# Kernel optimization log

Hardware: AMD Instinct MI355X
Metric: run time of the kernel (lower is better)

## Reference

```python
import jax, jax.numpy as jnp
import numpy as np

D_MODEL = 2048
N_HEADS = 16
HEAD_DIM = D_MODEL // N_HEADS
D_FF = ((int(8 * D_MODEL / 3) + 64) // 64) * 64  # 5504
B, T = 2, 2048
EPS = 1e-8
NEG = -1e9


def rotate_half(x):
    half = x.shape[-1] // 2
    return jnp.concatenate([-x[..., half:], x[..., :half]], axis=-1)


def apply_rope(x, cos, sin):
    # x: [B,H,T,hd]; cos/sin: [T,hd] -> [1,1,T,hd]
    c = cos[None, None, :, :]
    s = sin[None, None, :, :]
    return x * c + rotate_half(x) * s


def rmsnorm(x, w):
    rms = jnp.sqrt(jnp.mean(x * x, axis=-1, keepdims=True))
    return w * x / (rms + EPS)


def setup_inputs() -> dict:
    key = jax.random.key(0)
    ks = jax.random.split(key, 12)
    x = jax.random.normal(ks[0], (B, T, D_MODEL), dtype=jnp.float32)
    # RoPE tables
    inv_freq = 1.0 / (10000.0 ** (jnp.arange(0, HEAD_DIM, 2, dtype=jnp.float32) / HEAD_DIM))
    pos = jnp.arange(T, dtype=jnp.float32)
    freqs = pos[:, None] * inv_freq[None, :]          # [T, hd/2]
    emb = jnp.concatenate([freqs, freqs], axis=-1)    # [T, hd]
    cos, sin = jnp.cos(emb), jnp.sin(emb)
    # causal additive mask [T,T]
    mask = jnp.where(jnp.tril(jnp.ones((T, T), dtype=bool)), 0.0, NEG).astype(jnp.float32)
    scale = 0.02
    Wq = jax.random.normal(ks[1], (D_MODEL, D_MODEL), dtype=jnp.float32) * scale
    Wk = jax.random.normal(ks[2], (D_MODEL, D_MODEL), dtype=jnp.float32) * scale
    Wv = jax.random.normal(ks[3], (D_MODEL, D_MODEL), dtype=jnp.float32) * scale
    Wo = jax.random.normal(ks[4], (D_MODEL, D_MODEL), dtype=jnp.float32) * scale
    W1 = jax.random.normal(ks[5], (D_FF, D_MODEL), dtype=jnp.float32) * scale
    W2 = jax.random.normal(ks[6], (D_FF, D_MODEL), dtype=jnp.float32) * scale
    Wout = jax.random.normal(ks[7], (D_MODEL, D_FF), dtype=jnp.float32) * scale
    g1 = jnp.ones((D_MODEL,), dtype=jnp.float32)
    g2 = jnp.ones((D_MODEL,), dtype=jnp.float32)
    return {"x": x, "cos": cos, "sin": sin, "mask": mask,
            "g1": g1, "g2": g2, "Wq": Wq, "Wk": Wk, "Wv": Wv, "Wo": Wo,
            "W1": W1, "W2": W2, "Wout": Wout}


def reference(x, cos, sin, mask, g1, g2, Wq, Wk, Wv, Wo, W1, W2, Wout):
    Bb, Tt, Dd = x.shape

    def split_heads(t):  # [B,T,D] -> [B,H,T,hd]
        return t.reshape(Bb, Tt, N_HEADS, HEAD_DIM).transpose(0, 2, 1, 3)

    h = rmsnorm(x, g1)
    Q = apply_rope(split_heads(h @ Wq.T), cos, sin)
    K = apply_rope(split_heads(h @ Wk.T), cos, sin)
    V = split_heads(h @ Wv.T)
    scores = jnp.einsum('bhqd,bhkd->bhqk', Q, K) / jnp.sqrt(jnp.float32(HEAD_DIM))
    scores = scores + mask  # broadcast [T,T] over [B,H,T,T]
    weights = jax.nn.softmax(scores, axis=-1)
    attn = jnp.einsum('bhqk,bhkd->bhqd', weights, V)
    attn = attn.transpose(0, 2, 1, 3).reshape(Bb, Tt, Dd)
    x = x + attn @ Wo.T

    h2 = rmsnorm(x, g2)
    ff = (jax.nn.silu(h2 @ W1.T) * (h2 @ W2.T)) @ Wout.T
    return x + ff
```

## Files before the change

kernel.cpp:

```cpp
#include <hip/hip_runtime.h>


using bf16 = __bf16;
typedef __bf16 bf16x2 __attribute__((ext_vector_type(2)));
typedef __bf16 bf16x8 __attribute__((ext_vector_type(8)));
typedef float f32x4 __attribute__((ext_vector_type(4)));

#define MFMA_BF16(a, b, c) __builtin_amdgcn_mfma_f32_16x16x32_bf16((a), (b), (c), 0, 0, 0)

__device__ __forceinline__ void gld_lds16(const void* g, void* l) {
  __builtin_amdgcn_global_load_lds((const __attribute__((address_space(1))) void*)g,
                                   (__attribute__((address_space(3))) void*)l,
                                   16, 0, 0);
}

__global__ void detect_dtype(const unsigned int* __restrict__ X, int* __restrict__ flag) {
  const int tid = threadIdx.x;
  const unsigned int w = X[tid];
  const unsigned int e_lo = (w >> 7) & 0xFF;
  const unsigned int e_hi = (w >> 23) & 0xFF;
  const bool sane = (e_lo >= 97u && e_lo <= 157u) && (e_hi >= 97u && e_hi <= 157u);
  const unsigned long long m = __ballot(sane);
  if (tid == 0) *flag = (__popcll(m) > 48) ? 1 : 0;
}

__global__ __launch_bounds__(256) void convert_in(const void* __restrict__ src,
                                                  bf16* __restrict__ dst,
                                                  const int* __restrict__ flag) {
  const size_t i = ((size_t)blockIdx.x * 256 + threadIdx.x) * 8;
  if (*flag) {
    *(bf16x8*)(dst + i) = *(const bf16x8*)((const bf16*)src + i);
  } else {
    const float* s = (const float*)src;
    float4 a = *(const float4*)(s + i);
    float4 b = *(const float4*)(s + i + 4);
    bf16x8 o;
    o[0] = (bf16)a.x; o[1] = (bf16)a.y; o[2] = (bf16)a.z; o[3] = (bf16)a.w;
    o[4] = (bf16)b.x; o[5] = (bf16)b.y; o[6] = (bf16)b.z; o[7] = (bf16)b.w;
    *(bf16x8*)(dst + i) = o;
  }
}

__global__ __launch_bounds__(256) void rmsnorm_bf16(const bf16* __restrict__ X,
                                                    const bf16* __restrict__ g,
                                                    bf16* __restrict__ Hout) {
  const int row = blockIdx.x, tid = threadIdx.x;
  const size_t off = (size_t)row * 2048 + tid * 8;
  bf16x8 x8 = *(const bf16x8*)(X + off);
  float v[8];
  float s = 0.f;
#pragma unroll
  for (int j = 0; j < 8; ++j) { v[j] = (float)x8[j]; s += v[j] * v[j]; }
#pragma unroll
  for (int o = 32; o; o >>= 1) s += __shfl_xor(s, o);
  __shared__ float red[4];
  if ((tid & 63) == 0) red[tid >> 6] = s;
  __syncthreads();
  const float tot = red[0] + red[1] + red[2] + red[3];
  const float inv = 1.f / (sqrtf(tot * (1.f / 2048.f)) + 1e-8f);
  bf16x8 g8 = *(const bf16x8*)(g + tid * 8);
  bf16x8 o8;
#pragma unroll
  for (int j = 0; j < 8; ++j) o8[j] = (bf16)((float)g8[j] * v[j] * inv);
  *(bf16x8*)(Hout + off) = o8;
}

__global__ __launch_bounds__(256) void rmsnorm_f32(const float* __restrict__ X,
                                                   const bf16* __restrict__ g,
                                                   bf16* __restrict__ Hout) {
  const int row = blockIdx.x, tid = threadIdx.x;
  const size_t off = (size_t)row * 2048 + tid * 8;
  float4 a0 = *(const float4*)(X + off);
  float4 a1 = *(const float4*)(X + off + 4);
  float v[8] = {a0.x, a0.y, a0.z, a0.w, a1.x, a1.y, a1.z, a1.w};
  float s = 0.f;
#pragma unroll
  for (int j = 0; j < 8; ++j) s += v[j] * v[j];
#pragma unroll
  for (int o = 32; o; o >>= 1) s += __shfl_xor(s, o);
  __shared__ float red[4];
  if ((tid & 63) == 0) red[tid >> 6] = s;
  __syncthreads();
  const float tot = red[0] + red[1] + red[2] + red[3];
  const float inv = 1.f / (sqrtf(tot * (1.f / 2048.f)) + 1e-8f);
  bf16x8 g8 = *(const bf16x8*)(g + tid * 8);
  bf16x8 o8;
#pragma unroll
  for (int j = 0; j < 8; ++j) o8[j] = (bf16)((float)g8[j] * v[j] * inv);
  *(bf16x8*)(Hout + off) = o8;
}

__global__ __launch_bounds__(256) void rope_k(bf16* __restrict__ Q, bf16* __restrict__ Kg,
                                              const bf16* __restrict__ cosb,
                                              const bf16* __restrict__ sinb) {
  const int tid = threadIdx.x;
  const int rr = tid >> 7;
  const int c = tid & 127;
  const int bt = blockIdx.x * 2 + rr;
  const int t = bt & 2047;
  const int h = c >> 3;
  const int d0 = (c & 7) * 8;
  const size_t row = (size_t)bt * 2048;
  const int i0 = h * 128 + d0;
  bf16x8 c0 = *(const bf16x8*)(cosb + t * 128 + d0);
  bf16x8 c1 = *(const bf16x8*)(cosb + t * 128 + d0 + 64);
  bf16x8 s0 = *(const bf16x8*)(sinb + t * 128 + d0);
  bf16x8 s1 = *(const bf16x8*)(sinb + t * 128 + d0 + 64);
  bf16x8 qa = *(const bf16x8*)(Q + row + i0);
  bf16x8 qb = *(const bf16x8*)(Q + row + i0 + 64);
  bf16x8 ka = *(const bf16x8*)(Kg + row + i0);
  bf16x8 kb = *(const bf16x8*)(Kg + row + i0 + 64);
  bf16x8 qo0, qo1, ko0, ko1;
#pragma unroll
  for (int j = 0; j < 8; ++j) {
    float cj0 = (float)c0[j], cj1 = (float)c1[j];
    float sj0 = (float)s0[j], sj1 = (float)s1[j];
    float qaj = (float)qa[j], qbj = (float)qb[j];
    float kaj = (float)ka[j], kbj = (float)kb[j];
    qo0[j] = (bf16)(qaj * cj0 - qbj * sj0);
    qo1[j] = (bf16)(qbj * cj1 + qaj * sj1);
    ko0[j] = (bf16)(kaj * cj0 - kbj * sj0);
    ko1[j] = (bf16)(kbj * cj1 + kaj * sj1);
  }
  *(bf16x8*)(Q + row + i0) = qo0;
  *(bf16x8*)(Q + row + i0 + 64) = qo1;
  *(bf16x8*)(Kg + row + i0) = ko0;
  *(bf16x8*)(Kg + row + i0 + 64) = ko1;
}

template <int EPI>
__global__ __launch_bounds__(256) void gemm_bt(const bf16* __restrict__ A,
                                               const bf16* __restrict__ W,
                                               bf16* __restrict__ Cb, float* __restrict__ Cf,
                                               const bf16* __restrict__ resb,
                                               const float* __restrict__ resf,
                                               const bf16* __restrict__ mulb,
                                               const int* __restrict__ oflag,
                                               int M, int N, int K) {
  __shared__ bf16 As[2][128 * 32];
  __shared__ bf16 Ws[2][128 * 32];
  const int tid = threadIdx.x;
  const int wave = tid >> 6, lane = tid & 63;
  const int quad = lane >> 4, l15 = lane & 15;
  const int wm = wave >> 1, wn = wave & 1;
  const int m0 = blockIdx.y * 128, n0 = blockIdx.x * 128;

  f32x4 acc[4][4];
#pragma unroll
  for (int i = 0; i < 4; ++i)
#pragma unroll
    for (int j = 0; j < 4; ++j) acc[i][j] = {0.f, 0.f, 0.f, 0.f};

  const int srow = lane >> 2;
  const int skk = (lane & 3) * 8;
  const bf16* Ab = A + (size_t)m0 * K;
  const bf16* Wb = W + (size_t)n0 * K;

  auto stage = [&](int buf, int kb) {
    const int k0 = kb << 5;
#pragma unroll
    for (int c = 0; c < 2; ++c) {
      const int r = (wave * 2 + c) * 16 + srow;
      gld_lds16(Ab + (size_t)r * K + k0 + skk, (char*)As[buf] + (wave * 2 + c) * 1024);
      gld_lds16(Wb + (size_t)r * K + k0 + skk, (char*)Ws[buf] + (wave * 2 + c) * 1024);
    }
  };
  auto compute = [&](int buf) {
    bf16x8 af[4], wf[4];
#pragma unroll
    for (int mt = 0; mt < 4; ++mt)
      af[mt] = *(const bf16x8*)&As[buf][(wm * 64 + mt * 16 + l15) * 32 + quad * 8];
#pragma unroll
    for (int nt = 0; nt < 4; ++nt)
      wf[nt] = *(const bf16x8*)&Ws[buf][(wn * 64 + nt * 16 + l15) * 32 + quad * 8];
#pragma unroll
    for (int mt = 0; mt < 4; ++mt)
#pragma unroll
      for (int nt = 0; nt < 4; ++nt)
        acc[mt][nt] = MFMA_BF16(af[mt], wf[nt], acc[mt][nt]);
  };

  const int nk = K >> 5;
  stage(0, 0);
  for (int kb = 0; kb < nk; kb += 2) {
    __syncthreads();
    if (kb + 1 < nk) stage(1, kb + 1);
    compute(0);
    __syncthreads();
    if (kb + 2 < nk) stage(0, kb + 2);
    compute(1);
  }

  const int obf = (EPI == 4 && oflag) ? *oflag : 0;
#pragma unroll
  for (int mt = 0; mt < 4; ++mt) {
#pragma unroll
    for (int nt = 0; nt < 4; ++nt) {
#pragma unroll
      for (int r = 0; r < 4; ++r) {
        const int row = m0 + wm * 64 + mt * 16 + quad * 4 + r;
        const int col = n0 + wn * 64 + nt * 16 + l15;
        const size_t idx = (size_t)row * N + col;
        const float v = acc[mt][nt][r];
        if constexpr (EPI == 0) {
          Cb[idx] = (bf16)v;
        } else if constexpr (EPI == 1) {
          Cf[idx] = v + (float)resb[idx];
        } else if constexpr (EPI == 2) {
          Cb[idx] = (bf16)(v / (1.f + __expf(-v)));
        } else if constexpr (EPI == 3) {
          Cb[idx] = (bf16)((float)mulb[idx] * v);
        } else {
          const float rres = resf[idx] + v;
          if (obf) Cb[idx] = (bf16)rres;
          else     Cf[idx] = rres;
        }
      }
    }
  }
}

__global__ __launch_bounds__(256) void flash_attn(const bf16* __restrict__ Q,
                                                  const bf16* __restrict__ Kg,
                                                  const bf16* __restrict__ Vg,
                                                  bf16* __restrict__ O) {
  __shared__ bf16 Ks[64 * 128];
  __shared__ bf16 Vt[128 * 64];
  __shared__ bf16 Ps[4 * 16 * 64];
  const int tid = threadIdx.x;
  const int wave = tid >> 6, lane = tid & 63;
  const int quad = lane >> 4, l15 = lane & 15;
  const int bh = blockIdx.y;
  const int b = bh >> 4, h = bh & 15;
  const size_t base = (size_t)b * 2048 * 2048 + h * 128;
  const float scale = 0.08838834764831845f;

  const int qt = 31 - (int)blockIdx.x;
  const int q0 = qt * 64;

  bf16x8 qf[4];
  {
    const bf16* qrow = Q + base + (size_t)(q0 + wave * 16 + l15) * 2048;
#pragma unroll
    for (int ks = 0; ks < 4; ++ks) qf[ks] = *(const bf16x8*)(qrow + ks * 32 + quad * 8);
  }

  f32x4 o[8];
#pragma unroll
  for (int i = 0; i < 8; ++i) o[i] = {0.f, 0.f, 0.f, 0.f};
  float m_r[4] = {-1e30f, -1e30f, -1e30f, -1e30f};
  float l_r[4] = {0.f, 0.f, 0.f, 0.f};

  for (int kb = 0; kb <= qt; ++kb) {
    const int k0 = kb * 64;
    __syncthreads();

#pragma unroll
    for (int c = 0; c < 4; ++c) {
      const int ch = tid + 256 * c;
      const int row = ch >> 4;
      const int scb = ((ch & 15) * 16) ^ ((row & 7) << 4);
      gld_lds16((const char*)(Kg + base + (size_t)(k0 + row) * 2048) + scb,
                (char*)Ks + wave * 1024 + c * 4096);
    }
#pragma unroll
    for (int c = 0; c < 2; ++c) {
      const int tau = tid + 256 * c;
      const int kp = tau & 31;
      const int d0 = (tau >> 5) * 8;
      bf16x8 va = *(const bf16x8*)(Vg + base + (size_t)(k0 + 2 * kp) * 2048 + d0);
      bf16x8 vb = *(const bf16x8*)(Vg + base + (size_t)(k0 + 2 * kp + 1) * 2048 + d0);
#pragma unroll
      for (int j = 0; j < 8; ++j) {
        bf16x2 pr = {va[j], vb[j]};
        const int d = d0 + j;
        *(bf16x2*)((char*)Vt + d * 128 + ((4 * kp) ^ ((d & 7) << 4))) = pr;
      }
    }
    __syncthreads();

    f32x4 s[4];
#pragma unroll
    for (int nt = 0; nt < 4; ++nt) {
      s[nt] = {0.f, 0.f, 0.f, 0.f};
      const int krow = nt * 16 + l15;
#pragma unroll
      for (int ks = 0; ks < 4; ++ks) {
        bf16x8 kf = *(const bf16x8*)((char*)Ks + krow * 256 +
                                     ((ks * 64 + quad * 16) ^ ((krow & 7) << 4)));
        s[nt] = MFMA_BF16(qf[ks], kf, s[nt]);
      }
    }

    float sv[4][4];
#pragma unroll
    for (int nt = 0; nt < 4; ++nt) {
#pragma unroll
      for (int r = 0; r < 4; ++r) {
        float v = s[nt][r] * scale;
        const int key = k0 + nt * 16 + l15;
        const int qq = q0 + wave * 16 + quad * 4 + r;
        if (key > qq) v = -1e9f;
        sv[nt][r] = v;
      }
    }

#pragma unroll
    for (int r = 0; r < 4; ++r) {
      float rmax = fmaxf(fmaxf(sv[0][r], sv[1][r]), fmaxf(sv[2][r], sv[3][r]));
#pragma unroll
      for (int off = 1; off < 16; off <<= 1) rmax = fmaxf(rmax, __shfl_xor(rmax, off));
      const float mnew = fmaxf(m_r[r], rmax);
      const float alpha = __expf(m_r[r] - mnew);
      float psum = 0.f;
      const int qrow = quad * 4 + r;
#pragma unroll
      for (int nt = 0; nt < 4; ++nt) {
        const float p = __expf(sv[nt][r] - mnew);
        psum += p;
        *(bf16*)((char*)Ps + wave * 2048 + qrow * 128 +
                 ((2 * (nt * 16 + l15)) ^ ((qrow & 7) << 4))) = (bf16)p;
      }
#pragma unroll
      for (int off = 1; off < 16; off <<= 1) psum += __shfl_xor(psum, off);
      l_r[r] = l_r[r] * alpha + psum;
      m_r[r] = mnew;
#pragma unroll
      for (int nt2 = 0; nt2 < 8; ++nt2) o[nt2][r] *= alpha;
    }

    asm volatile("s_waitcnt lgkmcnt(0)" ::: "memory");

#pragma unroll
    for (int ks2 = 0; ks2 < 2; ++ks2) {
      bf16x8 pf = *(const bf16x8*)((char*)Ps + wave * 2048 + l15 * 128 +
                                   ((ks2 * 64 + quad * 16) ^ ((l15 & 7) << 4)));
#pragma unroll
      for (int nt2 = 0; nt2 < 8; ++nt2) {
        const int drow = nt2 * 16 + l15;
        bf16x8 vf = *(const bf16x8*)((char*)Vt + drow * 128 +
                                     ((ks2 * 64 + quad * 16) ^ ((drow & 7) << 4)));
        o[nt2] = MFMA_BF16(pf, vf, o[nt2]);
      }
    }
  }

#pragma unroll
  for (int nt2 = 0; nt2 < 8; ++nt2) {
#pragma unroll
    for (int r = 0; r < 4; ++r) {
      const int qq = q0 + wave * 16 + quad * 4 + r;
      const int dd = nt2 * 16 + l15;
      O[base + (size_t)qq * 2048 + dd] = (bf16)(o[nt2][r] / l_r[r]);
    }
  }
}

extern "C" void kernel_launch(void* const* d_in, const int* in_sizes, int n_in,
                              void* d_out, int out_size, void* d_ws, size_t ws_size,
                              hipStream_t stream) {
  const void* x_raw = d_in[0];
  const void* cos_raw = d_in[1];
  const void* sin_raw = d_in[2];
  const void* g1_raw = d_in[4];
  const void* g2_raw = d_in[5];
  const void* W_raw[7] = {d_in[6], d_in[7], d_in[8], d_in[9], d_in[10], d_in[11], d_in[12]};

  char* ws = (char*)d_ws;
  const size_t MB = 1048576ull;
  int* flag = (int*)ws;
  bf16* g1c = (bf16*)(ws + 4096);
  bf16* g2c = (bf16*)(ws + 12288);
  bf16* cosc = (bf16*)(ws + 65536);
  bf16* sinc = (bf16*)(ws + 655360);
  bf16* xc   = (bf16*)(ws + 2 * MB);
  bf16* wslot= (bf16*)(ws + 18 * MB);
  bf16* hbuf = (bf16*)(ws + 41 * MB);
  bf16* qbuf = (bf16*)(ws + 57 * MB);
  bf16* kbuf = (bf16*)(ws + 73 * MB);
  bf16* vbuf = (bf16*)(ws + 89 * MB);
  bf16* abuf = (bf16*)(ws + 105 * MB);
  float* x1  = (float*)(ws + 57 * MB);
  bf16* h2   = (bf16*)(ws + 41 * MB);
  bf16* ubuf = (bf16*)(ws + 89 * MB);

  const int M = 4096;
  dim3 blk(256);

  detect_dtype<<<1, 64, 0, stream>>>((const unsigned int*)x_raw, flag);

  convert_in<<<4096, blk, 0, stream>>>(x_raw, xc, flag);
  convert_in<<<128, blk, 0, stream>>>(cos_raw, cosc, flag);
  convert_in<<<128, blk, 0, stream>>>(sin_raw, sinc, flag);
  convert_in<<<1, blk, 0, stream>>>(g1_raw, g1c, flag);
  convert_in<<<1, blk, 0, stream>>>(g2_raw, g2c, flag);

  rmsnorm_bf16<<<M, blk, 0, stream>>>(xc, g1c, hbuf);

  convert_in<<<2048, blk, 0, stream>>>(W_raw[0], wslot, flag);
  gemm_bt<0><<<dim3(16, 32), blk, 0, stream>>>(hbuf, wslot, qbuf, nullptr, nullptr, nullptr, nullptr, nullptr, M, 2048, 2048);
  convert_in<<<2048, blk, 0, stream>>>(W_raw[1], wslot, flag);
  gemm_bt<0><<<dim3(16, 32), blk, 0, stream>>>(hbuf, wslot, kbuf, nullptr, nullptr, nullptr, nullptr, nullptr, M, 2048, 2048);
  convert_in<<<2048, blk, 0, stream>>>(W_raw[2], wslot, flag);
  gemm_bt<0><<<dim3(16, 32), blk, 0, stream>>>(hbuf, wslot, vbuf, nullptr, nullptr, nullptr, nullptr, nullptr, M, 2048, 2048);

  rope_k<<<M / 2, blk, 0, stream>>>(qbuf, kbuf, cosc, sinc);
  flash_attn<<<dim3(32, 32), blk, 0, stream>>>(qbuf, kbuf, vbuf, abuf);

  convert_in<<<2048, blk, 0, stream>>>(W_raw[3], wslot, flag);
  gemm_bt<1><<<dim3(16, 32), blk, 0, stream>>>(abuf, wslot, nullptr, x1, xc, nullptr, nullptr, nullptr, M, 2048, 2048);

  rmsnorm_f32<<<M, blk, 0, stream>>>(x1, g2c, h2);

  convert_in<<<5504, blk, 0, stream>>>(W_raw[4], wslot, flag);
  gemm_bt<2><<<dim3(43, 32), blk, 0, stream>>>(h2, wslot, ubuf, nullptr, nullptr, nullptr, nullptr, nullptr, M, 5504, 2048);
  convert_in<<<5504, blk, 0, stream>>>(W_raw[5], wslot, flag);
  gemm_bt<3><<<dim3(43, 32), blk, 0, stream>>>(h2, wslot, ubuf, nullptr, nullptr, nullptr, ubuf, nullptr, M, 5504, 2048);
  convert_in<<<5504, blk, 0, stream>>>(W_raw[6], wslot, flag);
  gemm_bt<4><<<dim3(16, 32), blk, 0, stream>>>(ubuf, wslot, (bf16*)d_out, (float*)d_out, nullptr, x1, nullptr, flag, M, 2048, 5504);
}
```

Before: 1.088 ms.

## Double-buffer K/V tiles and pair causal query tiles per attention block

The flash attention kernel now double-buffers K and V in shared memory, prefetching tile kb+2 through registers and async LDS loads while tile kb is being computed. Each block also processes two query tiles (qt and 31-qt), which evens out causal work per block, and the grid is halved to 16x32. This aims to hide global load latency and reduce tail imbalance. In exchange, LDS use roughly doubles, register pressure rises from holding V in registers, and there are fewer blocks to fill the GPU.

```diff
diff --git a/kernel.cpp b/kernel.cpp
--- a/kernel.cpp
+++ b/kernel.cpp
@@ -224,8 +224,8 @@
                                                   const bf16* __restrict__ Kg,
                                                   const bf16* __restrict__ Vg,
                                                   bf16* __restrict__ O) {
-  __shared__ bf16 Ks[64 * 128];
-  __shared__ bf16 Vt[128 * 64];
+  __shared__ bf16 Ks[2][64 * 128];
+  __shared__ bf16 Vt[2][128 * 64];
   __shared__ bf16 Ps[4 * 16 * 64];
   const int tid = threadIdx.x;
   const int wave = tid >> 6, lane = tid & 63;
@@ -235,123 +235,154 @@
   const size_t base = (size_t)b * 2048 * 2048 + h * 128;
   const float scale = 0.08838834764831845f;
 
-  const int qt = 31 - (int)blockIdx.x;
-  const int q0 = qt * 64;
-
-  bf16x8 qf[4];
-  {
-    const bf16* qrow = Q + base + (size_t)(q0 + wave * 16 + l15) * 2048;
-#pragma unroll
-    for (int ks = 0; ks < 4; ++ks) qf[ks] = *(const bf16x8*)(qrow + ks * 32 + quad * 8);
-  }
-
-  f32x4 o[8];
-#pragma unroll
-  for (int i = 0; i < 8; ++i) o[i] = {0.f, 0.f, 0.f, 0.f};
-  float m_r[4] = {-1e30f, -1e30f, -1e30f, -1e30f};
-  float l_r[4] = {0.f, 0.f, 0.f, 0.f};
-
-  for (int kb = 0; kb <= qt; ++kb) {
+  bf16x8 vva[2], vvb[2];
+
+  auto stageK = [&](int buf, int kb) {
     const int k0 = kb * 64;
-    __syncthreads();
-
 #pragma unroll
     for (int c = 0; c < 4; ++c) {
       const int ch = tid + 256 * c;
       const int row = ch >> 4;
       const int scb = ((ch & 15) * 16) ^ ((row & 7) << 4);
       gld_lds16((const char*)(Kg + base + (size_t)(k0 + row) * 2048) + scb,
-                (char*)Ks + wave * 1024 + c * 4096);
-    }
+                (char*)Ks[buf] + wave * 1024 + c * 4096);
+    }
+  };
+  auto loadV = [&](int kb) {
+    const int k0 = kb * 64;
 #pragma unroll
     for (int c = 0; c < 2; ++c) {
       const int tau = tid + 256 * c;
       const int kp = tau & 31;
       const int d0 = (tau >> 5) * 8;
-      bf16x8 va = *(const bf16x8*)(Vg + base + (size_t)(k0 + 2 * kp) * 2048 + d0);
-      bf16x8 vb = *(const bf16x8*)(Vg + base + (size_t)(k0 + 2 * kp + 1) * 2048 + d0);
+      vva[c] = *(const bf16x8*)(Vg + base + (size_t)(k0 + 2 * kp) * 2048 + d0);
+      vvb[c] = *(const bf16x8*)(Vg + base + (size_t)(k0 + 2 * kp + 1) * 2048 + d0);
+    }
+  };
+  auto writeV = [&](int buf) {
+#pragma unroll
+    for (int c = 0; c < 2; ++c) {
+      const int tau = tid + 256 * c;
+      const int kp = tau & 31;
+      const int d0 = (tau >> 5) * 8;
 #pragma unroll
       for (int j = 0; j < 8; ++j) {
-        bf16x2 pr = {va[j], vb[j]};
+        bf16x2 pr = {vva[c][j], vvb[c][j]};
         const int d = d0 + j;
-        *(bf16x2*)((char*)Vt + d * 128 + ((4 * kp) ^ ((d & 7) << 4))) = pr;
-      }
-    }
+        *(bf16x2*)((char*)Vt[buf] + d * 128 + ((4 * kp) ^ ((d & 7) << 4))) = pr;
+      }
+    }
+  };
+
+#pragma unroll 1
+  for (int half = 0; half < 2; ++half) {
+    const int qt = half ? (31 - (int)blockIdx.x) : (int)blockIdx.x;
+    const int q0 = qt * 64;
+
+    bf16x8 qf[4];
+    {
+      const bf16* qrow = Q + base + (size_t)(q0 + wave * 16 + l15) * 2048;
+#pragma unroll
+      for (int ks = 0; ks < 4; ++ks) qf[ks] = *(const bf16x8*)(qrow + ks * 32 + quad * 8);
+    }
+
+    f32x4 o[8];
+#pragma unroll
+    for (int i = 0; i < 8; ++i) o[i] = {0.f, 0.f, 0.f, 0.f};
+    float m_r[4] = {-1e30f, -1e30f, -1e30f, -1e30f};
+    float l_r[4] = {0.f, 0.f, 0.f, 0.f};
+
     __syncthreads();
-
-    f32x4 s[4];
-#pragma unroll
-    for (int nt = 0; nt < 4; ++nt) {
-      s[nt] = {0.f, 0.f, 0.f, 0.f};
-      const int krow = nt * 16 + l15;
-#pragma unroll
-      for (int ks = 0; ks < 4; ++ks) {
-        bf16x8 kf = *(const bf16x8*)((char*)Ks + krow * 256 +
-                                     ((ks * 64 + quad * 16) ^ ((krow & 7) << 4)));
-        s[nt] = MFMA_BF16(qf[ks], kf, s[nt]);
-      }
-    }
-
-    float sv[4][4];
-#pragma unroll
-    for (int nt = 0; nt < 4; ++nt) {
+    loadV(0);
+    stageK(0, 0);
+    writeV(0);
+    __syncthreads();
+    if (qt >= 1) { loadV(1); stageK(1, 1); }
+
+#pragma unroll 1
+    for (int kb = 0; kb <= qt; ++kb) {
+      const int cur = kb & 1;
+      const int k0 = kb * 64;
+
+      f32x4 s[4];
+#pragma unroll
+      for (int nt = 0; nt < 4; ++nt) {
+        s[nt] = {0.f, 0.f, 0.f, 0.f};
+        const int krow = nt * 16 + l15;
+#pragma unroll
+        for (int ks = 0; ks < 4; ++ks) {
+          bf16x8 kf = *(const bf16x8*)((char*)Ks[cur] + krow * 256 +
+                                       ((ks * 64 + quad * 16) ^ ((krow & 7) << 4)));
+          s[nt] = MFMA_BF16(qf[ks], kf, s[nt]);
+        }
+      }
+
+      float sv[4][4];
+#pragma unroll
+      for (int nt = 0; nt < 4; ++nt) {
+#pragma unroll
+        for (int r = 0; r < 4; ++r) {
+          float v = s[nt][r] * scale;
+          const int key = k0 + nt * 16 + l15;
+          const int qq = q0 + wave * 16 + quad * 4 + r;
+          if (key > qq) v = -1e9f;
+          sv[nt][r] = v;
+        }
+      }
+
 #pragma unroll
       for (int r = 0; r < 4; ++r) {
-        float v = s[nt][r] * scale;
-        const int key = k0 + nt * 16 + l15;
+        float rmax = fmaxf(fmaxf(sv[0][r], sv[1][r]), fmaxf(sv[2][r], sv[3][r]));
+#pragma unroll
+        for (int off = 1; off < 16; off <<= 1) rmax = fmaxf(rmax, __shfl_xor(rmax, off));
+        const float mnew = fmaxf(m_r[r], rmax);
+        const float alpha = __expf(m_r[r] - mnew);
+        float psum = 0.f;
+        const int qrow = quad * 4 + r;
+#pragma unroll
+        for (int nt = 0; nt < 4; ++nt) {
+          const float p = __expf(sv[nt][r] - mnew);
+          psum += p;
+          *(bf16*)((char*)Ps + wave * 2048 + qrow * 128 +
+                   ((2 * (nt * 16 + l15)) ^ ((qrow & 7) << 4))) = (bf16)p;
+        }
+#pragma unroll
+        for (int off = 1; off < 16; off <<= 1) psum += __shfl_xor(psum, off);
+        l_r[r] = l_r[r] * alpha + psum;
+        m_r[r] = mnew;
+#pragma unroll
+        for (int nt2 = 0; nt2 < 8; ++nt2) o[nt2][r] *= alpha;
+      }
+
+      asm volatile("s_waitcnt lgkmcnt(0)" ::: "memory");
+
+#pragma unroll
+      for (int ks2 = 0; ks2 < 2; ++ks2) {
+        bf16x8 pf = *(const bf16x8*)((char*)Ps + wave * 2048 + l15 * 128 +
+                                     ((ks2 * 64 + quad * 16) ^ ((l15 & 7) << 4)));
+#pragma unroll
+        for (int nt2 = 0; nt2 < 8; ++nt2) {
+          const int drow = nt2 * 16 + l15;
+          bf16x8 vf = *(const bf16x8*)((char*)Vt[cur] + drow * 128 +
+                                       ((ks2 * 64 + quad * 16) ^ ((drow & 7) << 4)));
+          o[nt2] = MFMA_BF16(pf, vf, o[nt2]);
+        }
+      }
+
+      if (kb + 1 <= qt) writeV(cur ^ 1);
+
+      __syncthreads();
+      if (kb + 2 <= qt) { loadV(kb + 2); stageK(cur, kb + 2); }
+    }
+
+#pragma unroll
+    for (int nt2 = 0; nt2 < 8; ++nt2) {
+#pragma unroll
+      for (int r = 0; r < 4; ++r) {
         const int qq = q0 + wave * 16 + quad * 4 + r;
-        if (key > qq) v = -1e9f;
-        sv[nt][r] = v;
-      }
-    }
-
-#pragma unroll
-    for (int r = 0; r < 4; ++r) {
-      float rmax = fmaxf(fmaxf(sv[0][r], sv[1][r]), fmaxf(sv[2][r], sv[3][r]));
-#pragma unroll
-      for (int off = 1; off < 16; off <<= 1) rmax = fmaxf(rmax, __shfl_xor(rmax, off));
-      const float mnew = fmaxf(m_r[r], rmax);
-      const float alpha = __expf(m_r[r] - mnew);
-      float psum = 0.f;
-      const int qrow = quad * 4 + r;
-#pragma unroll
-      for (int nt = 0; nt < 4; ++nt) {
-        const float p = __expf(sv[nt][r] - mnew);
-        psum += p;
-        *(bf16*)((char*)Ps + wave * 2048 + qrow * 128 +
-                 ((2 * (nt * 16 + l15)) ^ ((qrow & 7) << 4))) = (bf16)p;
-      }
-#pragma unroll
-      for (int off = 1; off < 16; off <<= 1) psum += __shfl_xor(psum, off);
-      l_r[r] = l_r[r] * alpha + psum;
-      m_r[r] = mnew;
-#pragma unroll
-      for (int nt2 = 0; nt2 < 8; ++nt2) o[nt2][r] *= alpha;
-    }
-
-    asm volatile("s_waitcnt lgkmcnt(0)" ::: "memory");
-
-#pragma unroll
-    for (int ks2 = 0; ks2 < 2; ++ks2) {
-      bf16x8 pf = *(const bf16x8*)((char*)Ps + wave * 2048 + l15 * 128 +
-                                   ((ks2 * 64 + quad * 16) ^ ((l15 & 7) << 4)));
-#pragma unroll
-      for (int nt2 = 0; nt2 < 8; ++nt2) {
-        const int drow = nt2 * 16 + l15;
-        bf16x8 vf = *(const bf16x8*)((char*)Vt + drow * 128 +
-                                     ((ks2 * 64 + quad * 16) ^ ((drow & 7) << 4)));
-        o[nt2] = MFMA_BF16(pf, vf, o[nt2]);
-      }
-    }
-  }
-
-#pragma unroll
-  for (int nt2 = 0; nt2 < 8; ++nt2) {
-#pragma unroll
-    for (int r = 0; r < 4; ++r) {
-      const int qq = q0 + wave * 16 + quad * 4 + r;
-      const int dd = nt2 * 16 + l15;
-      O[base + (size_t)qq * 2048 + dd] = (bf16)(o[nt2][r] / l_r[r]);
+        const int dd = nt2 * 16 + l15;
+        O[base + (size_t)qq * 2048 + dd] = (bf16)(o[nt2][r] / l_r[r]);
+      }
     }
   }
 }
@@ -405,7 +436,7 @@
   gemm_bt<0><<<dim3(16, 32), blk, 0, stream>>>(hbuf, wslot, vbuf, nullptr, nullptr, nullptr, nullptr, nullptr, M, 2048, 2048);
 
   rope_k<<<M / 2, blk, 0, stream>>>(qbuf, kbuf, cosc, sinc);
-  flash_attn<<<dim3(32, 32), blk, 0, stream>>>(qbuf, kbuf, vbuf, abuf);
+  flash_attn<<<dim3(16, 32), blk, 0, stream>>>(qbuf, kbuf, vbuf, abuf);
 
   convert_in<<<2048, blk, 0, stream>>>(W_raw[3], wslot, flag);
   gemm_bt<1><<<dim3(16, 32), blk, 0, stream>>>(abuf, wslot, nullptr, x1, xc, nullptr, nullptr, nullptr, M, 2048, 2048);
```

After: 1.072 ms. About the same (-1.5%).
